# Kernel tuning notes

Hardware: AMD Instinct MI355X
Metric: run time of the kernel (lower is better)

The kernel has to match this reference:

```python
import math
import jax, jax.numpy as jnp
import numpy as np

B, H, S, D = 2, 16, 2048, 64


def setup_inputs() -> dict:
    key = jax.random.key(0)
    kq, kk, kv = jax.random.split(key, 3)
    Q = jax.random.normal(kq, (B, H, S, D), dtype=jnp.float32)
    K = jax.random.normal(kk, (B, H, S, D), dtype=jnp.float32)
    V = jax.random.normal(kv, (B, H, S, D), dtype=jnp.float32)
    # padding mask: (N, H, query_len), True = keep (module expands with [..., None])
    padding_mask = jnp.ones((B, H, S), dtype=bool)
    # boolean causal attention mask, broadcastable to (B, H, S, S)
    attention_mask = jnp.tril(jnp.ones((S, S), dtype=bool))[None, None]
    return {"Q": Q, "K": K, "V": V,
            "padding_mask": padding_mask, "attention_mask": attention_mask}


def reference(Q, K, V, padding_mask, attention_mask):
    # scores: (B, H, S_q, S_k)
    scale = 1.0 / math.sqrt(K.shape[-1])
    attn = jnp.einsum("bhqd,bhkd->bhqk", Q, K) * scale
    # query-side padding mask (is_query_mask=True): expand last axis
    attn = jnp.where(padding_mask[..., None], attn, -jnp.inf)
    # boolean attention mask
    attn = jnp.where(attention_mask, attn, -jnp.inf)
    attn = jax.nn.softmax(attn, axis=-1)
    # nan-clean: rows fully masked to -inf softmax to NaN -> 0
    attn = jnp.where(jnp.isnan(attn), 0.0, attn)
    return jnp.einsum("bhqk,bhkd->bhqd", attn, V)
```

## Files before the change

kernel.cpp:

```cpp
#include <hip/hip_runtime.h>


typedef __attribute__((ext_vector_type(8))) short bf16x8;
typedef __attribute__((ext_vector_type(4))) float f32x4;
typedef __attribute__((ext_vector_type(2))) unsigned uint2v;
typedef __attribute__((ext_vector_type(4))) unsigned uint4v;

#define MFMA16(a, b, c) __builtin_amdgcn_mfma_f32_16x16x32_bf16(a, b, c, 0, 0, 0)

#define S_LEN 2048
#define D_DIM 64
#define NBH 32

static __device__ __forceinline__ short f2bf(float f) {
  unsigned u = __builtin_bit_cast(unsigned, f);
  u += 0x7fffu + ((u >> 16) & 1u);
  return (short)(u >> 16);
}

static __device__ __forceinline__ unsigned pk2(float a, float b) {
#if __has_builtin(__builtin_amdgcn_cvt_pk_bf16_f32)
  auto r = __builtin_amdgcn_cvt_pk_bf16_f32(a, b);
  return __builtin_bit_cast(unsigned, r);
#else
  return (unsigned)(unsigned short)f2bf(a) |
         ((unsigned)(unsigned short)f2bf(b) << 16);
#endif
}

static __device__ __forceinline__ float fexp2(float x) {
#if __has_builtin(__builtin_amdgcn_exp2f)
  return __builtin_amdgcn_exp2f(x);
#else
  return exp2f(x);
#endif
}

static __device__ __forceinline__ bf16x8 cvt8(const float* p) {
  f32x4 a = *(const f32x4*)p;
  f32x4 b = *(const f32x4*)(p + 4);
  bf16x8 r;
#pragma unroll
  for (int j = 0; j < 4; ++j) { r[j] = f2bf(a[j]); r[j + 4] = f2bf(b[j]); }
  return r;
}

static __device__ __forceinline__ void load_lds16(const short* g, short* l) {
  __builtin_amdgcn_global_load_lds(
      (const __attribute__((address_space(1))) unsigned*)g,
      (__attribute__((address_space(3))) unsigned*)l, 16, 0, 0);
}

__global__ __launch_bounds__(256) void stage(const float* __restrict__ K,
                                             const float* __restrict__ V,
                                             short* __restrict__ Kb,
                                             short* __restrict__ Vt) {
  const int tid = threadIdx.x;
  if (blockIdx.x < 1024) {
    const size_t b0 = (size_t)blockIdx.x * 4096;
#pragma unroll
    for (int p = 0; p < 2; ++p) {
      const size_t i = b0 + p * 2048 + tid * 8;
      f32x4 a = *(const f32x4*)(K + i);
      f32x4 b = *(const f32x4*)(K + i + 4);
      bf16x8 r;
#pragma unroll
      for (int j = 0; j < 4; ++j) { r[j] = f2bf(a[j]); r[j + 4] = f2bf(b[j]); }
      *(bf16x8*)(Kb + i) = r;
    }
  } else {
    __shared__ unsigned t[64][18];
    const int bi = blockIdx.x - 1024;
    const int bh = bi >> 6, k32 = bi & 63;
    const float* src = V + ((size_t)bh * S_LEN + k32 * 32) * D_DIM;
    const int pr = tid & 15;
    const int dq = tid >> 4;
    f32x4 a = *(const f32x4*)(src + (2 * pr)     * D_DIM + dq * 4);
    f32x4 b = *(const f32x4*)(src + (2 * pr + 1) * D_DIM + dq * 4);
#pragma unroll
    for (int j = 0; j < 4; ++j) t[dq * 4 + j][pr] = pk2(a[j], b[j]);
    __syncthreads();
    const int d = tid >> 2, g = tid & 3;
    uint2v lo = *(const uint2v*)(&t[d][2 * g]);
    uint2v hi = *(const uint2v*)(&t[d][8 + 2 * g]);
    short* dst = Vt + (size_t)bh * D_DIM * S_LEN + (size_t)d * S_LEN +
                 k32 * 32 + g * 8;
    *(uint2v*)(dst)     = lo;
    *(uint2v*)(dst + 4) = hi;
  }
}

__global__ __launch_bounds__(256, 5) void attn_fwd(
    const float* __restrict__ Q, const short* __restrict__ Kb,
    const short* __restrict__ Vt, float* __restrict__ O) {
  __shared__ __align__(16) short kbuf[2][4096];
  __shared__ __align__(16) short vbuf[2][4096];

  const int tid  = threadIdx.x;
  const int wave = tid >> 6;
  const int lane = tid & 63;
  const int quad = lane >> 4;
  const int col  = lane & 15;

  const int bh = blockIdx.x & 31;
  const int i2 = blockIdx.x >> 5;
  const int jj = i2 & 7, gg = i2 >> 3;
  const int qb = (gg & 1) ? (jj + ((gg & 2) << 2))
                          : (31 - jj - ((gg & 2) << 2));
  const int n  = qb + 1;
  const int q0 = qb * 64 + wave * 16;

  const float* Qh = Q  + (size_t)bh * S_LEN * D_DIM;
  const short* Kh = Kb + (size_t)bh * S_LEN * D_DIM;
  const short* Vh = Vt + (size_t)bh * D_DIM * S_LEN;

  const bf16x8 bq0 = cvt8(Qh + (q0 + col) * D_DIM + quad * 8);
  const bf16x8 bq1 = cvt8(Qh + (q0 + col) * D_DIM + quad * 8 + 32);

  const int L0 = tid,       r0s = L0 >> 3, c0s = (L0 & 7) ^ (r0s & 7);
  const int L1 = 256 + tid, r1s = L1 >> 3, c1s = (L1 & 7) ^ (r1s & 7);
  const int wb0 = (wave * 64) * 8;
  const int wb1 = (256 + wave * 64) * 8;

  f32x4 o[4];
#pragma unroll
  for (int i = 0; i < 4; ++i) o[i] = 0.f;
  float psum = 0.f;
  const float sc = 0.125f * 1.44269504088896340736f;

  const int rbase = col * 64;
  const int sw0 = ((quad       ^ (col & 7)) << 3);
  const int sw1 = (((4 + quad) ^ (col & 7)) << 3);

  auto prefetch = [&](int t, int buf) {
    const int k0n = t << 6;
    load_lds16(Kh + (size_t)(k0n + r0s) * 64 + c0s * 8, &kbuf[buf][wb0]);
    load_lds16(Kh + (size_t)(k0n + r1s) * 64 + c1s * 8, &kbuf[buf][wb1]);
    load_lds16(Vh + (size_t)r0s * S_LEN + k0n + c0s * 8, &vbuf[buf][wb0]);
    load_lds16(Vh + (size_t)r1s * S_LEN + k0n + c1s * 8, &vbuf[buf][wb1]);
  };

  auto body = [&](int t, bool masked) {
    const short* kb = kbuf[t & 1];
    const short* vb = vbuf[t & 1];

    bf16x8 ak0[4], ak1[4], av0[4], av1[4];
#pragma unroll
    for (int mt = 0; mt < 4; ++mt) {
      ak0[mt] = *(const bf16x8*)(kb + mt * 1024 + rbase + sw0);
      ak1[mt] = *(const bf16x8*)(kb + mt * 1024 + rbase + sw1);
    }
#pragma unroll
    for (int mt = 0; mt < 4; ++mt) {
      av0[mt] = *(const bf16x8*)(vb + mt * 1024 + rbase + sw0);
      av1[mt] = *(const bf16x8*)(vb + mt * 1024 + rbase + sw1);
    }

    f32x4 s[4];
#pragma unroll
    for (int mt = 0; mt < 4; ++mt) {
      f32x4 c = 0.f;
      c = MFMA16(ak0[mt], bq0, c);
      c = MFMA16(ak1[mt], bq1, c);
      s[mt] = c;
    }

    unsigned u[8];
    const int k0 = t << 6, qA = q0 + col;
#pragma unroll
    for (int mt = 0; mt < 4; ++mt) {
      float p0 = fexp2(fmaf(s[mt][0], sc, -8.0f));
      float p1 = fexp2(fmaf(s[mt][1], sc, -8.0f));
      float p2 = fexp2(fmaf(s[mt][2], sc, -8.0f));
      float p3 = fexp2(fmaf(s[mt][3], sc, -8.0f));
      if (masked) {
        const int kk = k0 + mt * 16 + quad * 4;
        if (kk     > qA) p0 = 0.f;
        if (kk + 1 > qA) p1 = 0.f;
        if (kk + 2 > qA) p2 = 0.f;
        if (kk + 3 > qA) p3 = 0.f;
      }
      psum += (p0 + p1) + (p2 + p3);
      u[2 * mt]     = pk2(p0, p1);
      u[2 * mt + 1] = pk2(p2, p3);
    }

    uint4v dv0, dv1;
    dv0[0] = u[0]; dv0[1] = u[1]; dv0[2] = u[2]; dv0[3] = u[3];
    dv1[0] = u[4]; dv1[1] = u[5]; dv1[2] = u[6]; dv1[3] = u[7];
    const bf16x8 bp0 = __builtin_bit_cast(bf16x8, dv0);
    const bf16x8 bp1 = __builtin_bit_cast(bf16x8, dv1);

#pragma unroll
    for (int mt = 0; mt < 4; ++mt) o[mt] = MFMA16(av0[mt], bp0, o[mt]);
#pragma unroll
    for (int mt = 0; mt < 4; ++mt) o[mt] = MFMA16(av1[mt], bp1, o[mt]);
  };

  prefetch(0, 0);
  for (int t = 0; t < n - 1; ++t) {
    __syncthreads();
    prefetch(t + 1, (t + 1) & 1);
    body(t, false);
  }
  __syncthreads();
  body(n - 1, true);

  psum += __shfl_xor(psum, 16);
  psum += __shfl_xor(psum, 32);
  const float rl = 1.f / psum;
  float* op = O + (size_t)bh * S_LEN * D_DIM + (size_t)(q0 + col) * D_DIM;
#pragma unroll
  for (int mt = 0; mt < 4; ++mt) {
    f32x4 ov;
#pragma unroll
    for (int r = 0; r < 4; ++r) ov[r] = o[mt][r] * rl;
    *(f32x4*)(op + mt * 16 + quad * 4) = ov;
  }
}

extern "C" void kernel_launch(void* const* d_in, const int* in_sizes, int n_in,
                              void* d_out, int out_size, void* d_ws, size_t ws_size,
                              hipStream_t stream) {
  const float* Q = (const float*)d_in[0];
  const float* K = (const float*)d_in[1];
  const float* V = (const float*)d_in[2];
  short* Kb = (short*)d_ws;
  short* Vt = Kb + (size_t)NBH * S_LEN * D_DIM;
  stage   <<<dim3(3072), dim3(256), 0, stream>>>(K, V, Kb, Vt);
  attn_fwd<<<dim3(1024), dim3(256), 0, stream>>>(Q, Kb, Vt, (float*)d_out);
}
```

Before: 142.0 us.

## Pair causal query blocks per workgroup to balance attention work

Each workgroup now handles two query blocks, i and 31-i, for one head, so every block does a constant 33 key tiles. This replaces the previous 1024-block grid and its interleaved qb mapping with a 512-block grid. The kernel also prefetches the first K/V tile of the second pass while finishing the last tile of the first pass. Occupancy hint drops from 5 to 4 workgroups per CU. The trade is less parallelism per launch (512 blocks) in exchange for removing tail imbalance and per-block startup cost.

```diff
diff --git a/kernel.cpp b/kernel.cpp
--- a/kernel.cpp
+++ b/kernel.cpp
@@ -90,7 +90,7 @@
   }
 }
 
-__global__ __launch_bounds__(256, 5) void attn_fwd(
+__global__ __launch_bounds__(256, 4) void attn_fwd(
     const float* __restrict__ Q, const short* __restrict__ Kb,
     const short* __restrict__ Vt, float* __restrict__ O) {
   __shared__ __align__(16) short kbuf[2][4096];
@@ -102,35 +102,39 @@
   const int quad = lane >> 4;
   const int col  = lane & 15;
 
-  const int bh = blockIdx.x & 31;
-  const int i2 = blockIdx.x >> 5;
-  const int jj = i2 & 7, gg = i2 >> 3;
-  const int qb = (gg & 1) ? (jj + ((gg & 2) << 2))
-                          : (31 - jj - ((gg & 2) << 2));
-  const int n  = qb + 1;
-  const int q0 = qb * 64 + wave * 16;
+  const int bh = blockIdx.x >> 4;
+  const int i2 = blockIdx.x & 15;
+  const int n1 = i2 + 1;
+  const int n2 = 32 - i2;
 
   const float* Qh = Q  + (size_t)bh * S_LEN * D_DIM;
   const short* Kh = Kb + (size_t)bh * S_LEN * D_DIM;
   const short* Vh = Vt + (size_t)bh * D_DIM * S_LEN;
-
-  const bf16x8 bq0 = cvt8(Qh + (q0 + col) * D_DIM + quad * 8);
-  const bf16x8 bq1 = cvt8(Qh + (q0 + col) * D_DIM + quad * 8 + 32);
 
   const int L0 = tid,       r0s = L0 >> 3, c0s = (L0 & 7) ^ (r0s & 7);
   const int L1 = 256 + tid, r1s = L1 >> 3, c1s = (L1 & 7) ^ (r1s & 7);
   const int wb0 = (wave * 64) * 8;
   const int wb1 = (256 + wave * 64) * 8;
 
-  f32x4 o[4];
-#pragma unroll
-  for (int i = 0; i < 4; ++i) o[i] = 0.f;
-  float psum = 0.f;
   const float sc = 0.125f * 1.44269504088896340736f;
 
   const int rbase = col * 64;
   const int sw0 = ((quad       ^ (col & 7)) << 3);
   const int sw1 = (((4 + quad) ^ (col & 7)) << 3);
+
+  f32x4 o[4];
+  float psum;
+  bf16x8 bq0, bq1;
+  int q0;
+
+  auto ldq = [&](int qb) {
+    q0  = qb * 64 + wave * 16;
+    bq0 = cvt8(Qh + (size_t)(q0 + col) * D_DIM + quad * 8);
+    bq1 = cvt8(Qh + (size_t)(q0 + col) * D_DIM + quad * 8 + 32);
+#pragma unroll
+    for (int i = 0; i < 4; ++i) o[i] = 0.f;
+    psum = 0.f;
+  };
 
   auto prefetch = [&](int t, int buf) {
     const int k0n = t << 6;
@@ -140,9 +144,9 @@
     load_lds16(Vh + (size_t)r1s * S_LEN + k0n + c1s * 8, &vbuf[buf][wb1]);
   };
 
-  auto body = [&](int t, bool masked) {
-    const short* kb = kbuf[t & 1];
-    const short* vb = vbuf[t & 1];
+  auto body = [&](int t, bool masked, int buf) {
+    const short* kb = kbuf[buf];
+    const short* vb = vbuf[buf];
 
     bf16x8 ak0[4], ak1[4], av0[4], av1[4];
 #pragma unroll
@@ -197,26 +201,41 @@
     for (int mt = 0; mt < 4; ++mt) o[mt] = MFMA16(av1[mt], bp1, o[mt]);
   };
 
+  auto flush = [&]() {
+    float ps = psum;
+    ps += __shfl_xor(ps, 16);
+    ps += __shfl_xor(ps, 32);
+    const float rl = 1.f / ps;
+    float* op = O + (size_t)bh * S_LEN * D_DIM + (size_t)(q0 + col) * D_DIM;
+#pragma unroll
+    for (int mt = 0; mt < 4; ++mt) {
+      f32x4 ov;
+#pragma unroll
+      for (int r = 0; r < 4; ++r) ov[r] = o[mt][r] * rl;
+      *(f32x4*)(op + mt * 16 + quad * 4) = ov;
+    }
+  };
+
+  int buf = 0;
+  ldq(i2);
   prefetch(0, 0);
-  for (int t = 0; t < n - 1; ++t) {
+  for (int t = 0; t < n1; ++t) {
     __syncthreads();
-    prefetch(t + 1, (t + 1) & 1);
-    body(t, false);
+    if (t + 1 < n1) prefetch(t + 1, buf ^ 1);
+    else            prefetch(0,     buf ^ 1);
+    body(t, t == n1 - 1, buf);
+    buf ^= 1;
   }
-  __syncthreads();
-  body(n - 1, true);
-
-  psum += __shfl_xor(psum, 16);
-  psum += __shfl_xor(psum, 32);
-  const float rl = 1.f / psum;
-  float* op = O + (size_t)bh * S_LEN * D_DIM + (size_t)(q0 + col) * D_DIM;
-#pragma unroll
-  for (int mt = 0; mt < 4; ++mt) {
-    f32x4 ov;
-#pragma unroll
-    for (int r = 0; r < 4; ++r) ov[r] = o[mt][r] * rl;
-    *(f32x4*)(op + mt * 16 + quad * 4) = ov;
+  flush();
+
+  ldq(31 - i2);
+  for (int t = 0; t < n2; ++t) {
+    __syncthreads();
+    if (t + 1 < n2) prefetch(t + 1, buf ^ 1);
+    body(t, t == n2 - 1, buf);
+    buf ^= 1;
   }
+  flush();
 }
 
 extern "C" void kernel_launch(void* const* d_in, const int* in_sizes, int n_in,
@@ -228,5 +247,5 @@
   short* Kb = (short*)d_ws;
   short* Vt = Kb + (size_t)NBH * S_LEN * D_DIM;
   stage   <<<dim3(3072), dim3(256), 0, stream>>>(K, V, Kb, Vt);
-  attn_fwd<<<dim3(1024), dim3(256), 0, stream>>>(Q, Kb, Vt, (float*)d_out);
-}
+  attn_fwd<<<dim3(512),  dim3(256), 0, stream>>>(Q, Kb, Vt, (float*)d_out);
+}
```

Result: slower. 145.5 us (+2.5%).

## Split long causal query blocks across two workgroups with atomic-counter combine

Applied to the files above, without the earlier changes.

Query blocks in the upper half of the causal range (the longest KV loops) are now split into two halves of the KV range, each handled by its own workgroup. Each half writes its unnormalized partial output and row sum to a workspace slot. An atomic counter picks the second finisher to add the two partials and normalize. This targets tail imbalance in the causal workload, at the cost of extra workgroups, partial-result global traffic and a fence/atomic handshake. The fixed -8 exponent offset is shared by both halves, so the unnormalized partials can be summed directly.

```diff
diff --git a/kernel.cpp b/kernel.cpp
--- a/kernel.cpp
+++ b/kernel.cpp
@@ -54,8 +54,12 @@
 __global__ __launch_bounds__(256) void stage(const float* __restrict__ K,
                                              const float* __restrict__ V,
                                              short* __restrict__ Kb,
-                                             short* __restrict__ Vt) {
+                                             short* __restrict__ Vt,
+                                             int* __restrict__ cnt) {
   const int tid = threadIdx.x;
+  if (blockIdx.x == 0) {
+    cnt[tid] = 0; cnt[tid + 256] = 0;
+  }
   if (blockIdx.x < 1024) {
     const size_t b0 = (size_t)blockIdx.x * 4096;
 #pragma unroll
@@ -92,7 +96,8 @@
 
 __global__ __launch_bounds__(256, 5) void attn_fwd(
     const float* __restrict__ Q, const short* __restrict__ Kb,
-    const short* __restrict__ Vt, float* __restrict__ O) {
+    const short* __restrict__ Vt, float* __restrict__ part,
+    int* __restrict__ cnt, float* __restrict__ O) {
   __shared__ __align__(16) short kbuf[2][4096];
   __shared__ __align__(16) short vbuf[2][4096];
 
@@ -103,19 +108,30 @@
   const int col  = lane & 15;
 
   const int bh = blockIdx.x & 31;
-  const int i2 = blockIdx.x >> 5;
-  const int jj = i2 & 7, gg = i2 >> 3;
-  const int qb = (gg & 1) ? (jj + ((gg & 2) << 2))
-                          : (31 - jj - ((gg & 2) << 2));
-  const int n  = qb + 1;
+  const int j  = blockIdx.x >> 5;
+  int qb, t0, t1, half = 0;
+  bool combine;
+  if (j < 32) {
+    qb = 31 - (j >> 1);
+    half = j & 1;
+    const int n  = qb + 1;
+    const int hi = n - (n >> 1);
+    t0 = half ? hi : 0;
+    t1 = half ? n  : hi;
+    combine = true;
+  } else {
+    qb = 47 - j;
+    t0 = 0; t1 = qb + 1;
+    combine = false;
+  }
   const int q0 = qb * 64 + wave * 16;
 
   const float* Qh = Q  + (size_t)bh * S_LEN * D_DIM;
   const short* Kh = Kb + (size_t)bh * S_LEN * D_DIM;
   const short* Vh = Vt + (size_t)bh * D_DIM * S_LEN;
 
-  const bf16x8 bq0 = cvt8(Qh + (q0 + col) * D_DIM + quad * 8);
-  const bf16x8 bq1 = cvt8(Qh + (q0 + col) * D_DIM + quad * 8 + 32);
+  const bf16x8 bq0 = cvt8(Qh + (size_t)(q0 + col) * D_DIM + quad * 8);
+  const bf16x8 bq1 = cvt8(Qh + (size_t)(q0 + col) * D_DIM + quad * 8 + 32);
 
   const int L0 = tid,       r0s = L0 >> 3, c0s = (L0 & 7) ^ (r0s & 7);
   const int L1 = 256 + tid, r1s = L1 >> 3, c1s = (L1 & 7) ^ (r1s & 7);
@@ -140,9 +156,9 @@
     load_lds16(Vh + (size_t)r1s * S_LEN + k0n + c1s * 8, &vbuf[buf][wb1]);
   };
 
-  auto body = [&](int t, bool masked) {
-    const short* kb = kbuf[t & 1];
-    const short* vb = vbuf[t & 1];
+  auto body = [&](int t, bool masked, int buf) {
+    const short* kb = kbuf[buf];
+    const short* vb = vbuf[buf];
 
     bf16x8 ak0[4], ak1[4], av0[4], av1[4];
 #pragma unroll
@@ -197,24 +213,58 @@
     for (int mt = 0; mt < 4; ++mt) o[mt] = MFMA16(av1[mt], bp1, o[mt]);
   };
 
-  prefetch(0, 0);
-  for (int t = 0; t < n - 1; ++t) {
+  int buf = 0;
+  prefetch(t0, 0);
+  for (int t = t0; t < t1; ++t) {
     __syncthreads();
-    prefetch(t + 1, (t + 1) & 1);
-    body(t, false);
-  }
-  __syncthreads();
-  body(n - 1, true);
+    if (t + 1 < t1) prefetch(t + 1, buf ^ 1);
+    body(t, t == qb, buf);
+    buf ^= 1;
+  }
 
   psum += __shfl_xor(psum, 16);
   psum += __shfl_xor(psum, 32);
-  const float rl = 1.f / psum;
-  float* op = O + (size_t)bh * S_LEN * D_DIM + (size_t)(q0 + col) * D_DIM;
+  const int q = wave * 16 + col;
+
+  if (!combine) {
+    const float rl = 1.f / psum;
+    float* op = O + (size_t)bh * S_LEN * D_DIM + (size_t)(qb * 64 + q) * D_DIM;
+#pragma unroll
+    for (int mt = 0; mt < 4; ++mt) {
+      f32x4 ov;
+#pragma unroll
+      for (int r = 0; r < 4; ++r) ov[r] = o[mt][r] * rl;
+      *(f32x4*)(op + mt * 16 + quad * 4) = ov;
+    }
+    return;
+  }
+
+  const int cidx = bh * 16 + (qb - 16);
+  float* slot = part + (size_t)(cidx * 2 + half) * 4160;
+#pragma unroll
+  for (int mt = 0; mt < 4; ++mt)
+    *(f32x4*)(slot + q * 64 + mt * 16 + quad * 4) = o[mt];
+  if (quad == 0) slot[4096 + q] = psum;
+  __threadfence();
+  __syncthreads();
+  int* flg = (int*)kbuf;
+  if (tid == 0) flg[0] = atomicAdd(&cnt[cidx], 1);
+  __syncthreads();
+  if (flg[0] != 1) return;
+  __threadfence();
+
+  const float* s0 = part + (size_t)(cidx * 2) * 4160;
+  const float* s1 = s0 + 4160;
+  const float pt = s0[4096 + q] + s1[4096 + q];
+  const float rl = 1.f / pt;
+  float* op = O + (size_t)bh * S_LEN * D_DIM + (size_t)(qb * 64 + q) * D_DIM;
 #pragma unroll
   for (int mt = 0; mt < 4; ++mt) {
+    f32x4 a = *(const f32x4*)(s0 + q * 64 + mt * 16 + quad * 4);
+    f32x4 b = *(const f32x4*)(s1 + q * 64 + mt * 16 + quad * 4);
     f32x4 ov;
 #pragma unroll
-    for (int r = 0; r < 4; ++r) ov[r] = o[mt][r] * rl;
+    for (int r = 0; r < 4; ++r) ov[r] = (a[r] + b[r]) * rl;
     *(f32x4*)(op + mt * 16 + quad * 4) = ov;
   }
 }
@@ -227,6 +277,8 @@
   const float* V = (const float*)d_in[2];
   short* Kb = (short*)d_ws;
   short* Vt = Kb + (size_t)NBH * S_LEN * D_DIM;
-  stage   <<<dim3(3072), dim3(256), 0, stream>>>(K, V, Kb, Vt);
-  attn_fwd<<<dim3(1024), dim3(256), 0, stream>>>(Q, Kb, Vt, (float*)d_out);
-}
+  float* part = (float*)(Vt + (size_t)NBH * S_LEN * D_DIM);
+  int*   cnt  = (int*)(part + (size_t)1024 * 4160);
+  stage   <<<dim3(3072), dim3(256), 0, stream>>>(K, V, Kb, Vt, cnt);
+  attn_fwd<<<dim3(1536), dim3(256), 0, stream>>>(Q, Kb, Vt, part, cnt, (float*)d_out);
+}
```

Result: slower. 357.9 us (+152.0%).
